# Performance work log

Hardware: AMD Instinct MI355X
Metric: run time of the kernel (lower is better)

The kernel has to match this reference:

```python
import jax, jax.numpy as jnp
import numpy as np
import math

FREQ_DIM = 161
OUTPUT_DIM = 4096
RNN_DIM = 128
EMBED_DIM = 32


def conv2d(x, w, b, stride):
    # x: (B, Cin, H, W), w: (Cout, Cin, kh, kw)
    out = jax.lax.conv_general_dilated(x, w, window_strides=stride, padding='VALID',
                                       dimension_numbers=('NCHW', 'OIHW', 'NCHW'))
    return out + b[None, :, None, None]


def gru_seq(x, w_ih, w_hh, b_ih, b_hh, h0):
    # x: (B, T, D); PyTorch GRU gate order: r, z, n
    B, T, D = x.shape
    H = h0.shape[-1]
    xg = jnp.einsum('btd,gd->btg', x, w_ih) + b_ih  # (B, T, 3H)

    def step(h, xg_t):
        hg = h @ w_hh.T + b_hh
        xr, xz, xn = jnp.split(xg_t, 3, axis=-1)
        hr, hz, hn = jnp.split(hg, 3, axis=-1)
        r = jax.nn.sigmoid(xr + hr)
        z = jax.nn.sigmoid(xz + hz)
        n = jnp.tanh(xn + r * hn)
        h_new = (1 - z) * n + z * h
        return h_new, h_new

    _, hs = jax.lax.scan(step, h0, jnp.swapaxes(xg, 0, 1))
    return jnp.swapaxes(hs, 0, 1)  # (B, T, H)


def gru_cell(ix, h, w_ih, w_hh, b_ih, b_hh):
    xg = ix @ w_ih.T + b_ih
    hg = h @ w_hh.T + b_hh
    xr, xz, xn = jnp.split(xg, 3, axis=-1)
    hr, hz, hn = jnp.split(hg, 3, axis=-1)
    r = jax.nn.sigmoid(xr + hr)
    z = jax.nn.sigmoid(xz + hz)
    n = jnp.tanh(xn + r * hn)
    return (1 - z) * n + z * h


def attend(eh, dhx):
    # eh: (B, T, H), dhx: (B, H)
    scores = jnp.einsum('bth,bh->bt', eh, dhx)
    a = jax.nn.softmax(scores, axis=-1)
    return jnp.einsum('bth,bt->bh', eh, a)


def setup_inputs() -> dict:
    key = jax.random.key(0)
    ks = jax.random.split(key, 16)

    def rn(k, shape, fan_in):
        s = 1.0 / math.sqrt(fan_in)
        return jax.random.uniform(k, shape, jnp.float32, -s, s)

    B, T_audio, L = 32, 512, 128
    x = jax.random.normal(ks[0], (B, T_audio, FREQ_DIM), jnp.float32)
    y = jax.random.randint(ks[1], (B, L), 0, OUTPUT_DIM)

    conv_in = 544  # 17 * 32 after two convs on freq dim 161
    params = {
        'conv1_w': rn(ks[2], (32, 1, 5, 32), 1 * 5 * 32),
        'conv1_b': rn(ks[3], (32,), 1 * 5 * 32),
        'conv2_w': rn(ks[4], (32, 32, 5, 32), 32 * 5 * 32),
        'conv2_b': rn(ks[5], (32,), 32 * 5 * 32),
        'rnn_w_ih': rn(ks[6], (3 * RNN_DIM, conv_in), RNN_DIM),
        'rnn_w_hh': rn(ks[7], (3 * RNN_DIM, RNN_DIM), RNN_DIM),
        'rnn_b_ih': rn(ks[8], (3 * RNN_DIM,), RNN_DIM),
        'rnn_b_hh': rn(ks[9], (3 * RNN_DIM,), RNN_DIM),
        'emb': jax.random.normal(ks[10], (OUTPUT_DIM, EMBED_DIM), jnp.float32),
        'dec_w_ih': rn(ks[11], (3 * RNN_DIM, EMBED_DIM), RNN_DIM),
        'dec_w_hh': rn(ks[12], (3 * RNN_DIM, RNN_DIM), RNN_DIM),
        'dec_b_ih': rn(ks[13], (3 * RNN_DIM,), RNN_DIM),
        'dec_b_hh': rn(ks[14], (3 * RNN_DIM,), RNN_DIM),
        'fc_w': rn(ks[15], (OUTPUT_DIM, RNN_DIM), RNN_DIM),
        'fc_b': rn(jax.random.fold_in(key, 99), (OUTPUT_DIM,), RNN_DIM),
        'h_init': jnp.zeros((1, RNN_DIM), jnp.float32),
    }
    return {'x': x, 'y': y, **params}


def forward(x, y, conv1_w, conv1_b, conv2_w, conv2_b,
            rnn_w_ih, rnn_w_hh, rnn_b_ih, rnn_b_hh,
            emb, dec_w_ih, dec_w_hh, dec_b_ih, dec_b_hh,
            fc_w, fc_b, h_init):
    B = x.shape[0]
    h = x[:, None, :, :]  # (B, 1, T, F)
    h = jax.nn.relu(conv2d(h, conv1_w, conv1_b, (2, 2)))
    h = jax.nn.relu(conv2d(h, conv2_w, conv2_b, (2, 2)))  # (B, 32, t, f)
    h = jnp.transpose(h, (0, 2, 3, 1))  # (B, t, f, c)
    b, t, f, c = h.shape
    h = h.reshape(b, t, f * c)
    eh = gru_seq(h, rnn_w_ih, rnn_w_hh, rnn_b_ih, rnn_b_hh,
                 jnp.zeros((b, RNN_DIM), h.dtype))  # (B, t, 128)

    inputs = emb[y[:, :-1]]  # (B, L-1, 32)
    hx = jnp.broadcast_to(h_init, (B, RNN_DIM))
    hx = hx + attend(eh, hx)

    def step(hx, ix):
        hx = gru_cell(ix, hx, dec_w_ih, dec_w_hh, dec_b_ih, dec_b_hh)
        hx = hx + attend(eh, hx)
        return hx, hx

    _, outs = jax.lax.scan(step, hx, jnp.swapaxes(inputs, 0, 1))
    out = jnp.concatenate([hx[:, None, :], jnp.swapaxes(outs, 0, 1)], axis=1)  # (B, L, 128)
    logits = jnp.einsum('btd,od->bto', out, fc_w) + fc_b
    return logits


def reference(x, y, conv1_w, conv1_b, conv2_w, conv2_b,
              rnn_w_ih, rnn_w_hh, rnn_b_ih, rnn_b_hh,
              emb, dec_w_ih, dec_w_hh, dec_b_ih, dec_b_hh,
              fc_w, fc_b, h_init):
    return forward(x, y, conv1_w, conv1_b, conv2_w, conv2_b,
                   rnn_w_ih, rnn_w_hh, rnn_b_ih, rnn_b_hh,
                   emb, dec_w_ih, dec_w_hh, dec_b_ih, dec_b_hh,
                   fc_w, fc_b, h_init)
```

## Files before the change

kernel.cpp:

```cpp
#include <hip/hip_runtime.h>
#include <stdint.h>

typedef unsigned short u16;
typedef uint32_t u32;

typedef __bf16 bf16x8 __attribute__((ext_vector_type(8)));
typedef float f32x4 __attribute__((ext_vector_type(4)));
typedef _Float16 h2v __attribute__((ext_vector_type(2)));

union B8 { uint4 q; u32 u[4]; bf16x8 v; };

__device__ __forceinline__ u16 f2bf(float f) {
  u32 u = __float_as_uint(f);
  u32 r = (u + 0x7fffu + ((u >> 16) & 1u)) >> 16;
  return (u16)r;
}
__device__ __forceinline__ u16 f2h(float f) {
  union { _Float16 h; u16 u; } v; v.h = (_Float16)f; return v.u;
}
__device__ __forceinline__ float dot2h(u32 a, u32 b, float c) {
  union U { u32 u; h2v v; } A, B; A.u = a; B.u = b;
  return __builtin_amdgcn_fdot2(A.v, B.v, c, false);
}
__device__ __forceinline__ float sigf(float x) { return 1.f / (1.f + __expf(-x)); }
__device__ __forceinline__ float tanhf_fast(float x) {
  x = fminf(fmaxf(x, -15.f), 15.f);
  float e = __expf(2.f * x);
  return (e - 1.f) / (e + 1.f);
}

__global__ __launch_bounds__(256) void prep_k(
    const float* rnn_w_hh, const float* dec_w_hh, const float* conv1_w,
    const float* conv2_w, const float* rnn_w_ih, const float* dec_w_ih,
    const float* fc_w, const float* emb, const int* y,
    u32* wT2e, u32* wT2d, u16* w1b, u16* w2b, u16* wihb, u16* dwihb,
    u16* fcwb, u16* adec)
{
  int e = blockIdx.x * 256 + threadIdx.x;
  const int S0 = 24576, S1 = 24576, S2 = 5120, S3 = 163840, S4 = 208896,
            S5 = 12288, S6 = 524288, S7 = 130048;
  if (e < S0) { int g = e >> 6, k2 = e & 63;
    wT2e[e] = (u32)f2h(rnn_w_hh[g*128 + 2*k2]) | ((u32)f2h(rnn_w_hh[g*128 + 2*k2 + 1]) << 16);
    return; }
  e -= S0;
  if (e < S1) { int g = e >> 6, k2 = e & 63;
    wT2d[e] = (u32)f2h(dec_w_hh[g*128 + 2*k2]) | ((u32)f2h(dec_w_hh[g*128 + 2*k2 + 1]) << 16);
    return; }
  e -= S1;
  if (e < S2) { int kh = e >> 10, c = (e >> 5) & 31, kw = e & 31;
    w1b[e] = f2bf(conv1_w[c*160 + kh*32 + kw]); return; }
  e -= S2;
  if (e < S3) { int kt = e >> 10, c = (e >> 5) & 31, kw = e & 31;
    int ic = kt / 5, kh = kt - ic * 5;
    w2b[e] = f2bf(conv2_w[((c*32 + ic)*5 + kh)*32 + kw]); return; }
  e -= S3;
  if (e < S4) { wihb[e] = f2bf(rnn_w_ih[e]); return; }
  e -= S4;
  if (e < S5) { dwihb[e] = f2bf(dec_w_ih[e]); return; }
  e -= S5;
  if (e < S6) { fcwb[e] = f2bf(fc_w[e]); return; }
  e -= S6;
  if (e < S7) { int m = e >> 5, k = e & 31;
    int b = m / 127, t = m - b * 127;
    adec[e] = f2bf(emb[y[b*128 + t]*32 + k]); return; }
}

__global__ __launch_bounds__(256) void conv1_k(const float* x, const u16* w1b,
                                               const float* c1b, u16* in1b)
{
  __shared__ __align__(16) u16 slab[35 * 162];
  __shared__ __align__(16) u16 wl[5120];
  int b = blockIdx.x >> 4;
  int oh0 = (blockIdx.x & 15) * 16;
  int ih0 = oh0 * 2;
  for (int e = threadIdx.x; e < 35 * 161; e += 256) {
    int r = e / 161, iw = e - r * 161;
    int ih = ih0 + r;
    float v = (ih < 512) ? x[(b*512 + ih)*161 + iw] : 0.f;
    slab[r*162 + iw] = f2bf(v);
  }
  for (int e = threadIdx.x; e < 5120; e += 256) wl[e] = w1b[e];
  __syncthreads();
  int lane = threadIdx.x & 63, wid = threadIdx.x >> 6;
  int lrow = lane & 15, lk = (lane >> 4) * 8;
  B8 bw[5][2];
  #pragma unroll
  for (int kt = 0; kt < 5; kt++)
    #pragma unroll
    for (int ct = 0; ct < 2; ct++)
      bw[kt][ct].q = *(const uint4*)&wl[(kt*32 + ct*16 + lrow)*32 + lk];
  float bias0 = c1b[lrow], bias1 = c1b[16 + lrow];
  for (int mt = wid; mt < 65; mt += 4) {
    int m = mt * 16 + lrow;
    int ohl = m / 65, ow = m - ohl * 65;
    int ro = ohl * 324 + ow * 2 + lk;
    f32x4 a0, a1;
    #pragma unroll
    for (int i = 0; i < 4; i++) { a0[i] = 0.f; a1[i] = 0.f; }
    #pragma unroll
    for (int kt = 0; kt < 5; kt++) {
      B8 af;
      const u32* p = (const u32*)&slab[ro + kt * 162];
      af.u[0] = p[0]; af.u[1] = p[1]; af.u[2] = p[2]; af.u[3] = p[3];
      a0 = __builtin_amdgcn_mfma_f32_16x16x32_bf16(af.v, bw[kt][0].v, a0, 0, 0, 0);
      a1 = __builtin_amdgcn_mfma_f32_16x16x32_bf16(af.v, bw[kt][1].v, a1, 0, 0, 0);
    }
    int rb = mt * 16 + (lane >> 4) * 4;
    #pragma unroll
    for (int i = 0; i < 4; i++) {
      int mr = rb + i;
      int ohl2 = mr / 65, ow2 = mr - ohl2 * 65;
      int oh = oh0 + ohl2;
      if (oh < 254) {
        float v0 = fmaxf(a0[i] + bias0, 0.f);
        float v1 = fmaxf(a1[i] + bias1, 0.f);
        in1b[((b*32 + lrow)*254 + oh)*72 + ow2] = f2bf(v0);
        in1b[((b*32 + 16 + lrow)*254 + oh)*72 + ow2] = f2bf(v1);
      }
    }
  }
}

__global__ __launch_bounds__(256) void conv2_k(const u16* in1b, const u16* w2b,
                                               const float* c2b, u16* hbf)
{
  extern __shared__ char smem[];
  u16* slab = (u16*)smem;
  u16* wl = (u16*)(smem + 87552);
  int b = blockIdx.x >> 4;
  int oh0 = (blockIdx.x & 15) * 8;
  int ih0 = oh0 * 2;
  for (int q = threadIdx.x; q < 5472; q += 256) {
    int ic = q / 171;
    int rem = q - ic * 171;
    int r = rem / 9, j = rem - r * 9;
    int ih = ih0 + r;
    uint4 v = make_uint4(0u, 0u, 0u, 0u);
    if (ih < 254) v = *(const uint4*)&in1b[(((b*32 + ic)*254 + ih)*72) + j*8];
    *(uint4*)&slab[(ic*19 + r)*72 + j*8] = v;
  }
  int lane = threadIdx.x & 63, wid = threadIdx.x >> 6;
  int lrow = lane & 15, lk = (lane >> 4) * 8;
  int ohl_[3], ow_[3];
  #pragma unroll
  for (int q = 0; q < 3; q++) {
    int mt = (q == 2) ? 8 : (wid + q * 4);
    int m = mt * 16 + lrow;
    if (m > 135) m = 0;
    ohl_[q] = m / 17; ow_[q] = m - ohl_[q] * 17;
  }
  f32x4 acc[3][2];
  #pragma unroll
  for (int q = 0; q < 3; q++)
    #pragma unroll
    for (int ct = 0; ct < 2; ct++)
      #pragma unroll
      for (int i = 0; i < 4; i++) acc[q][ct][i] = 0.f;

  for (int ph = 0; ph < 5; ph++) {
    __syncthreads();
    {
      const uint4* s4 = (const uint4*)&w2b[ph * 32768];
      uint4* d4 = (uint4*)wl;
      for (int q = threadIdx.x; q < 4096; q += 256) d4[q] = s4[q];
    }
    __syncthreads();
    for (int ktl = 0; ktl < 32; ktl++) {
      int ktg = ph * 32 + ktl;
      int ic = ktg / 5, kh = ktg - ic * 5;
      B8 fb0, fb1;
      fb0.q = *(const uint4*)&wl[(ktl*32 + lrow)*32 + lk];
      fb1.q = *(const uint4*)&wl[(ktl*32 + 16 + lrow)*32 + lk];
      int base = (ic * 19 + kh) * 72 + lk;
      #pragma unroll
      for (int q = 0; q < 3; q++) {
        if (q == 2 && wid != 0) break;
        B8 af;
        const u32* p = (const u32*)&slab[base + ohl_[q] * 144 + ow_[q] * 2];
        af.u[0] = p[0]; af.u[1] = p[1]; af.u[2] = p[2]; af.u[3] = p[3];
        acc[q][0] = __builtin_amdgcn_mfma_f32_16x16x32_bf16(af.v, fb0.v, acc[q][0], 0, 0, 0);
        acc[q][1] = __builtin_amdgcn_mfma_f32_16x16x32_bf16(af.v, fb1.v, acc[q][1], 0, 0, 0);
      }
    }
  }
  #pragma unroll
  for (int q = 0; q < 3; q++) {
    if (q == 2 && wid != 0) break;
    int mt = (q == 2) ? 8 : (wid + q * 4);
    int rb = mt * 16 + (lane >> 4) * 4;
    #pragma unroll
    for (int ct = 0; ct < 2; ct++) {
      int c = ct * 16 + lrow;
      float bias = c2b[c];
      #pragma unroll
      for (int i = 0; i < 4; i++) {
        int mr = rb + i;
        if (mr < 136) {
          int ohl = mr / 17, ow = mr - ohl * 17;
          int oh = oh0 + ohl;
          if (oh < 125) {
            float v = fmaxf(acc[q][ct][i] + bias, 0.f);
            hbf[(b*125 + oh)*544 + ow*32 + c] = f2bf(v);
          }
        }
      }
    }
  }
}

__global__ __launch_bounds__(256) void gemm_k(const u16* A, const u16* Bw,
                                              const float* bias, float* C,
                                              int M, int N, int K)
{
  __shared__ __align__(16) u16 As[64 * 32];
  __shared__ __align__(16) u16 Bs[64 * 32];
  int m0 = blockIdx.x * 64, n0 = blockIdx.y * 64;
  int tid = threadIdx.x;
  int lane = tid & 63, wid = tid >> 6;
  int lrow = lane & 15, lk = (lane >> 4) * 8;
  int sr = tid >> 2, sc8 = (tid & 3) * 8;
  f32x4 acc[4];
  #pragma unroll
  for (int nt = 0; nt < 4; nt++)
    #pragma unroll
    for (int i = 0; i < 4; i++) acc[nt][i] = 0.f;
  int nkt = K >> 5;
  for (int kt = 0; kt < nkt; kt++) {
    __syncthreads();
    uint4 va = make_uint4(0u, 0u, 0u, 0u);
    int arow = m0 + sr;
    if (arow < M) va = *(const uint4*)&A[arow * K + kt * 32 + sc8];
    *(uint4*)&As[sr * 32 + sc8] = va;
    uint4 vb = *(const uint4*)&Bw[(n0 + sr) * K + kt * 32 + sc8];
    *(uint4*)&Bs[sr * 32 + sc8] = vb;
    __syncthreads();
    B8 af; af.q = *(const uint4*)&As[(wid * 16 + lrow) * 32 + lk];
    #pragma unroll
    for (int nt = 0; nt < 4; nt++) {
      B8 bb; bb.q = *(const uint4*)&Bs[(nt * 16 + lrow) * 32 + lk];
      acc[nt] = __builtin_amdgcn_mfma_f32_16x16x32_bf16(af.v, bb.v, acc[nt], 0, 0, 0);
    }
  }
  #pragma unroll
  for (int nt = 0; nt < 4; nt++) {
    int col = n0 + nt * 16 + lrow;
    float bv = bias[col];
    #pragma unroll
    for (int i = 0; i < 4; i++) {
      int row = m0 + wid * 16 + (lane >> 4) * 4 + i;
      if (row < M) C[row * N + col] = acc[nt][i] + bv;
    }
  }
}

__global__ __launch_bounds__(1024, 1) void enc_k(const u32* wT2, const float* xg,
                                                 const float* bhh_g, u16* ehk, u16* eht)
{
  __shared__ __align__(16) u32 hp[2][2][64];
  __shared__ float hg[2][1152];
  int tid = threadIdx.x;
  int g = tid >> 9, tb = tid & 511, kh = tb >> 7, t = tb & 127;
  int b = blockIdx.x * 2 + g;
  u32 w0[16], w1[16], w2[16];
  {
    const uint4* p0 = (const uint4*)(wT2 + (size_t)t * 64 + kh * 16);
    const uint4* p1 = (const uint4*)(wT2 + (size_t)(128 + t) * 64 + kh * 16);
    const uint4* p2 = (const uint4*)(wT2 + (size_t)(256 + t) * 64 + kh * 16);
    #pragma unroll
    for (int j = 0; j < 4; j++) {
      uint4 q0 = p0[j]; w0[4*j] = q0.x; w0[4*j+1] = q0.y; w0[4*j+2] = q0.z; w0[4*j+3] = q0.w;
      uint4 q1 = p1[j]; w1[4*j] = q1.x; w1[4*j+1] = q1.y; w1[4*j+2] = q1.z; w1[4*j+3] = q1.w;
      uint4 q2 = p2[j]; w2[4*j] = q2.x; w2[4*j+1] = q2.y; w2[4*j+2] = q2.z; w2[4*j+3] = q2.w;
    }
  }
  float b0 = 0.f, b1 = 0.f, b2 = 0.f, xr0 = 0.f, xr1 = 0.f, xr2 = 0.f, hreg = 0.f;
  if (kh == 0) {
    b0 = bhh_g[t]; b1 = bhh_g[128 + t]; b2 = bhh_g[256 + t];
    const float* xp = &xg[(size_t)b * 125 * 384];
    xr0 = xp[t]; xr1 = xp[128 + t]; xr2 = xp[256 + t];
    ((u16*)&hp[g][0][0])[t] = 0;
  }
  __syncthreads();
  for (int tt = 0; tt < 125; tt++) {
    const u32* hb = &hp[g][tt & 1][kh * 16];
    float r0 = 0.f, r1 = 0.f, z0 = 0.f, z1 = 0.f, n0 = 0.f, n1 = 0.f;
    #pragma unroll
    for (int j = 0; j < 4; j++) {
      uint4 hv = *(const uint4*)&hb[4*j];
      r0 = dot2h(w0[4*j+0], hv.x, r0); r1 = dot2h(w0[4*j+1], hv.y, r1);
      r0 = dot2h(w0[4*j+2], hv.z, r0); r1 = dot2h(w0[4*j+3], hv.w, r1);
      z0 = dot2h(w1[4*j+0], hv.x, z0); z1 = dot2h(w1[4*j+1], hv.y, z1);
      z0 = dot2h(w1[4*j+2], hv.z, z0); z1 = dot2h(w1[4*j+3], hv.w, z1);
      n0 = dot2h(w2[4*j+0], hv.x, n0); n1 = dot2h(w2[4*j+1], hv.y, n1);
      n0 = dot2h(w2[4*j+2], hv.z, n0); n1 = dot2h(w2[4*j+3], hv.w, n1);
    }
    if (kh) {
      float* hh = &hg[g][(kh - 1) * 384];
      hh[t] = r0 + r1; hh[128 + t] = z0 + z1; hh[256 + t] = n0 + n1;
    }
    __syncthreads();
    if (kh == 0) {
      const float* hh = &hg[g][0];
      float pr = r0 + r1 + hh[t] + hh[384 + t] + hh[768 + t];
      float pz = z0 + z1 + hh[128 + t] + hh[512 + t] + hh[896 + t];
      float pn = n0 + n1 + hh[256 + t] + hh[640 + t] + hh[1024 + t];
      float r = sigf(xr0 + pr + b0);
      float z = sigf(xr1 + pz + b1);
      float n = tanhf_fast(xr2 + r * (pn + b2));
      hreg = (1.f - z) * n + z * hreg;
      u16 hv = f2h(hreg);
      ((u16*)&hp[g][(tt & 1) ^ 1][0])[t] = hv;
      ehk[((size_t)(b*64 + (t >> 1)) * 125 + tt) * 2 + (t & 1)] = hv;
      eht[((size_t)(b*128 + t)) * 128 + tt] = hv;
      if (tt + 1 < 125) {
        const float* xq = &xg[((size_t)b * 125 + tt + 1) * 384];
        xr0 = xq[t]; xr1 = xq[128 + t]; xr2 = xq[256 + t];
      }
    }
    __syncthreads();
  }
  if (kh == 0) {
    size_t rb = ((size_t)(b*128 + t)) * 128;
    eht[rb + 125] = 0; eht[rb + 126] = 0; eht[rb + 127] = 0;
  }
}

__global__ __launch_bounds__(1024, 1) void dec_k(const u32* wT2, const u32* ehk_g,
                                                 const u32* eht_g, const float* xgd,
                                                 const float* bhh_g, const float* h_init,
                                                 u16* outb)
{
  extern __shared__ char sm[];
  int tid = threadIdx.x;
  int g = tid >> 9, tb = tid & 511, kh = tb >> 7, t = tb & 127;
  int b = blockIdx.x * 2 + g;
  char* base = sm + (size_t)g * 41024;
  u32* elK   = (u32*)base;
  float* hgP = (float*)(base + 32000);
  float* sp  = (float*)(base + 36608);
  float* ctxB= (float*)(base + 38656);
  u16* hxA   = (u16*)(base + 40192);
  u16* hxB   = (u16*)(base + 40448);
  u16* scp   = (u16*)(base + 40704);
  float* red = (float*)(base + 40960);

  u32 w0[16], w1[16], w2[16];
  {
    const uint4* p0 = (const uint4*)(wT2 + (size_t)t * 64 + kh * 16);
    const uint4* p1 = (const uint4*)(wT2 + (size_t)(128 + t) * 64 + kh * 16);
    const uint4* p2 = (const uint4*)(wT2 + (size_t)(256 + t) * 64 + kh * 16);
    #pragma unroll
    for (int j = 0; j < 4; j++) {
      uint4 q0 = p0[j]; w0[4*j] = q0.x; w0[4*j+1] = q0.y; w0[4*j+2] = q0.z; w0[4*j+3] = q0.w;
      uint4 q1 = p1[j]; w1[4*j] = q1.x; w1[4*j+1] = q1.y; w1[4*j+2] = q1.z; w1[4*j+3] = q1.w;
      uint4 q2 = p2[j]; w2[4*j] = q2.x; w2[4*j+1] = q2.y; w2[4*j+2] = q2.z; w2[4*j+3] = q2.w;
    }
  }
  u32 rowr[16];
  {
    const uint4* rp = (const uint4*)(eht_g + (size_t)b * 8192 + (size_t)t * 64 + kh * 16);
    #pragma unroll
    for (int j = 0; j < 4; j++) {
      uint4 q = rp[j]; rowr[4*j] = q.x; rowr[4*j+1] = q.y; rowr[4*j+2] = q.z; rowr[4*j+3] = q.w;
    }
  }
  for (int e = tb; e < 8000; e += 512) elK[e] = ehk_g[(size_t)b * 8000 + e];
  float b0 = 0.f, b1 = 0.f, b2 = 0.f, xr0 = 0.f, xr1 = 0.f, xr2 = 0.f;
  float hxf = 0.f, hxg = 0.f;
  if (kh == 0) {
    b0 = bhh_g[t]; b1 = bhh_g[128 + t]; b2 = bhh_g[256 + t];
    hxf = h_init[t];
    const float* xp = &xgd[(size_t)b * 127 * 384];
    xr0 = xp[t]; xr1 = xp[128 + t]; xr2 = xp[256 + t];
  }
  __syncthreads();

  for (int step = 0; step < 128; step++) {
    if (step > 0) {
      const u32* hb = (const u32*)hxB + kh * 16;
      float r0 = 0.f, r1 = 0.f, z0 = 0.f, z1 = 0.f, n0 = 0.f, n1 = 0.f;
      #pragma unroll
      for (int j = 0; j < 4; j++) {
        uint4 hv = *(const uint4*)&hb[4*j];
        r0 = dot2h(w0[4*j+0], hv.x, r0); r1 = dot2h(w0[4*j+1], hv.y, r1);
        r0 = dot2h(w0[4*j+2], hv.z, r0); r1 = dot2h(w0[4*j+3], hv.w, r1);
        z0 = dot2h(w1[4*j+0], hv.x, z0); z1 = dot2h(w1[4*j+1], hv.y, z1);
        z0 = dot2h(w1[4*j+2], hv.z, z0); z1 = dot2h(w1[4*j+3], hv.w, z1);
        n0 = dot2h(w2[4*j+0], hv.x, n0); n1 = dot2h(w2[4*j+1], hv.y, n1);
        n0 = dot2h(w2[4*j+2], hv.z, n0); n1 = dot2h(w2[4*j+3], hv.w, n1);
      }
      if (kh) {
        float* hh = &hgP[(kh - 1) * 384];
        hh[t] = r0 + r1; hh[128 + t] = z0 + z1; hh[256 + t] = n0 + n1;
      }
      __syncthreads();
      if (kh == 0) {
        float pr = r0 + r1 + hgP[t] + hgP[384 + t] + hgP[768 + t];
        float pz = z0 + z1 + hgP[128 + t] + hgP[512 + t] + hgP[896 + t];
        float pn = n0 + n1 + hgP[256 + t] + hgP[640 + t] + hgP[1024 + t];
        float r = sigf(xr0 + pr + b0);
        float z = sigf(xr1 + pz + b1);
        float n = tanhf_fast(xr2 + r * (pn + b2));
        hxg = (1.f - z) * n + z * hxf;
        ((u16*)hxA)[t] = f2h(hxg);
        if (step < 127) {
          const float* xq = &xgd[((size_t)b * 127 + step) * 384];
          xr0 = xq[t]; xr1 = xq[128 + t]; xr2 = xq[256 + t];
        }
      }
      __syncthreads();
    } else {
      if (kh == 0) { hxg = hxf; ((u16*)hxA)[t] = f2h(hxg); }
      __syncthreads();
    }
    {
      float s0 = 0.f, s1 = 0.f;
      const u32* ek = &elK[(kh * 16) * 125];
      const u32* hxA4 = (const u32*)hxA;
      #pragma unroll
      for (int j = 0; j < 4; j++) {
        uint4 aw = *(const uint4*)&hxA4[kh * 16 + 4*j];
        s0 = dot2h(ek[(4*j+0)*125 + t], aw.x, s0);
        s1 = dot2h(ek[(4*j+1)*125 + t], aw.y, s1);
        s0 = dot2h(ek[(4*j+2)*125 + t], aw.z, s0);
        s1 = dot2h(ek[(4*j+3)*125 + t], aw.w, s1);
      }
      sp[kh * 128 + t] = s0 + s1;
    }
    __syncthreads();
    if (kh == 0) {
      float s = (t < 125) ? (sp[t] + sp[128 + t] + sp[256 + t] + sp[384 + t]) : -1e30f;
      float mw = s;
      #pragma unroll
      for (int o = 32; o > 0; o >>= 1) mw = fmaxf(mw, __shfl_xor(mw, o));
      float ev = (t < 125) ? __expf(s - mw) : 0.f;
      float sw = ev;
      #pragma unroll
      for (int o = 32; o > 0; o >>= 1) sw += __shfl_xor(sw, o);
      ((u16*)scp)[t] = f2h(ev);
      if ((t & 63) == 0) { int wv = t >> 6; red[wv*2] = mw; red[wv*2 + 1] = sw; }
    }
    __syncthreads();
    float m0r = red[0], S0r = red[1], m1r = red[2], S1r = red[3];
    float M = fmaxf(m0r, m1r);
    float f0 = __expf(m0r - M), f1 = __expf(m1r - M);
    float inv = 1.f / (f0 * S0r + f1 * S1r);
    float c0 = 0.f, c1 = 0.f;
    {
      const u32* scp4 = (const u32*)scp;
      #pragma unroll
      for (int j = 0; j < 4; j++) {
        uint4 sw4 = *(const uint4*)&scp4[kh * 16 + 4*j];
        c0 = dot2h(rowr[4*j+0], sw4.x, c0); c1 = dot2h(rowr[4*j+1], sw4.y, c1);
        c0 = dot2h(rowr[4*j+2], sw4.z, c0); c1 = dot2h(rowr[4*j+3], sw4.w, c1);
      }
    }
    if (kh) ctxB[(kh - 1) * 128 + t] = c0 + c1;
    __syncthreads();
    if (kh == 0) {
      float ctx = ((c0 + c1) + ctxB[t]) * f0 + (ctxB[128 + t] + ctxB[256 + t]) * f1;
      hxf = hxg + ctx * inv;
      outb[((size_t)(b * 128) + step) * 128 + t] = f2bf(hxf);
      ((u16*)hxB)[t] = f2h(hxf);
    }
    __syncthreads();
  }
}

extern "C" void kernel_launch(void* const* d_in, const int* in_sizes, int n_in,
                              void* d_out, int out_size, void* d_ws, size_t ws_size,
                              hipStream_t stream)
{
  const float* x        = (const float*)d_in[0];
  const int*   y        = (const int*)d_in[1];
  const float* conv1_w  = (const float*)d_in[2];
  const float* conv1_b  = (const float*)d_in[3];
  const float* conv2_w  = (const float*)d_in[4];
  const float* conv2_b  = (const float*)d_in[5];
  const float* rnn_w_ih = (const float*)d_in[6];
  const float* rnn_w_hh = (const float*)d_in[7];
  const float* rnn_b_ih = (const float*)d_in[8];
  const float* rnn_b_hh = (const float*)d_in[9];
  const float* emb      = (const float*)d_in[10];
  const float* dec_w_ih = (const float*)d_in[11];
  const float* dec_w_hh = (const float*)d_in[12];
  const float* dec_b_ih = (const float*)d_in[13];
  const float* dec_b_hh = (const float*)d_in[14];
  const float* fc_w     = (const float*)d_in[15];
  const float* fc_b     = (const float*)d_in[16];
  const float* h_init   = (const float*)d_in[17];
  float* logits = (float*)d_out;

  char* ws = (char*)d_ws;
  size_t off = 0;
  auto alloc = [&](size_t bytes) { char* p = ws + off; off = (off + bytes + 255) & ~(size_t)255; return p; };
  u16* in1b  = (u16*)alloc(37453824);
  u16* hbf   = (u16*)alloc(4352000);
  float* xge = (float*)alloc(6144000);
  u32* ehb_k = (u32*)alloc(1024000);
  u32* ehb_t = (u32*)alloc(1048576);
  float* xgd = (float*)alloc(6242304);
  u16* adec  = (u16*)alloc(260096);
  u16* outb  = (u16*)alloc(1048576);
  u32* wT2e  = (u32*)alloc(98304);
  u32* wT2d  = (u32*)alloc(98304);
  u16* w1b   = (u16*)alloc(10240);
  u16* w2b   = (u16*)alloc(327680);
  u16* wihb  = (u16*)alloc(417792);
  u16* dwihb = (u16*)alloc(24576);
  u16* fcwb  = (u16*)alloc(1048576);

  hipFuncSetAttribute((const void*)conv2_k, hipFuncAttributeMaxDynamicSharedMemorySize, 153088);
  hipFuncSetAttribute((const void*)dec_k,   hipFuncAttributeMaxDynamicSharedMemorySize, 82048);

  prep_k<<<4272, 256, 0, stream>>>(rnn_w_hh, dec_w_hh, conv1_w, conv2_w, rnn_w_ih,
                                   dec_w_ih, fc_w, emb, y,
                                   wT2e, wT2d, w1b, w2b, wihb, dwihb, fcwb, adec);
  conv1_k<<<512, 256, 0, stream>>>(x, w1b, conv1_b, in1b);
  conv2_k<<<512, 256, 153088, stream>>>(in1b, w2b, conv2_b, hbf);
  gemm_k<<<dim3(63, 6), 256, 0, stream>>>(hbf, wihb, rnn_b_ih, xge, 4000, 384, 544);
  gemm_k<<<dim3(64, 6), 256, 0, stream>>>(adec, dwihb, dec_b_ih, xgd, 4064, 384, 32);
  enc_k<<<16, 1024, 0, stream>>>(wT2e, xge, rnn_b_hh, (u16*)ehb_k, (u16*)ehb_t);
  dec_k<<<16, 1024, 82048, stream>>>(wT2d, ehb_k, ehb_t, xgd, dec_b_hh, h_init, outb);
  gemm_k<<<dim3(64, 64), 256, 0, stream>>>(outb, fcwb, fc_b, logits, 4096, 4096, 128);
}
```

Before: 604.0 us.

## Retile conv2 for more blocks, add dedicated FC GEMM, grid-stride prep kernel

conv2 now processes 4 output rows per block instead of 8 and stages weights in 10-row phases, which halves shared memory and doubles the block count to raise occupancy. The final logits projection moves from the generic 64x64 GEMM to a specialised 128x64 tile kernel that reuses B fragments across two M sub-tiles. The prep kernel processes four elements per thread with a quarter of the blocks. Smaller conv2 tiles add halo reloads and more weight-staging syncs.

After: 601.7 us (median of 2 runs). Within noise of the previous version (-0.4%).

```diff
diff --git a/kernel.cpp b/kernel.cpp
--- a/kernel.cpp
+++ b/kernel.cpp
@@ -29,14 +29,13 @@
   return (e - 1.f) / (e + 1.f);
 }
 
-__global__ __launch_bounds__(256) void prep_k(
+__device__ __forceinline__ void prep_one(int e,
     const float* rnn_w_hh, const float* dec_w_hh, const float* conv1_w,
     const float* conv2_w, const float* rnn_w_ih, const float* dec_w_ih,
     const float* fc_w, const float* emb, const int* y,
     u32* wT2e, u32* wT2d, u16* w1b, u16* w2b, u16* wihb, u16* dwihb,
     u16* fcwb, u16* adec)
 {
-  int e = blockIdx.x * 256 + threadIdx.x;
   const int S0 = 24576, S1 = 24576, S2 = 5120, S3 = 163840, S4 = 208896,
             S5 = 12288, S6 = 524288, S7 = 130048;
   if (e < S0) { int g = e >> 6, k2 = e & 63;
@@ -65,6 +64,23 @@
     adec[e] = f2bf(emb[y[b*128 + t]*32 + k]); return; }
 }
 
+__global__ __launch_bounds__(256) void prep_k(
+    const float* rnn_w_hh, const float* dec_w_hh, const float* conv1_w,
+    const float* conv2_w, const float* rnn_w_ih, const float* dec_w_ih,
+    const float* fc_w, const float* emb, const int* y,
+    u32* wT2e, u32* wT2d, u16* w1b, u16* w2b, u16* wihb, u16* dwihb,
+    u16* fcwb, u16* adec)
+{
+  int e0 = blockIdx.x * 256 + threadIdx.x;
+  #pragma unroll
+  for (int it = 0; it < 4; it++) {
+    int e = e0 + it * 273408;
+    if (e < 1093632)
+      prep_one(e, rnn_w_hh, dec_w_hh, conv1_w, conv2_w, rnn_w_ih, dec_w_ih,
+               fc_w, emb, y, wT2e, wT2d, w1b, w2b, wihb, dwihb, fcwb, adec);
+  }
+}
+
 __global__ __launch_bounds__(256) void conv1_k(const float* x, const u16* w1b,
                                                const float* c1b, u16* in1b)
 {
@@ -126,55 +142,56 @@
 {
   extern __shared__ char smem[];
   u16* slab = (u16*)smem;
-  u16* wl = (u16*)(smem + 87552);
-  int b = blockIdx.x >> 4;
-  int oh0 = (blockIdx.x & 15) * 8;
+  u16* wl = (u16*)(smem + 50688);
+  int b = blockIdx.x >> 5;
+  int tile = blockIdx.x & 31;
+  int oh0 = tile * 4;
   int ih0 = oh0 * 2;
-  for (int q = threadIdx.x; q < 5472; q += 256) {
-    int ic = q / 171;
-    int rem = q - ic * 171;
+  for (int q = threadIdx.x; q < 3168; q += 256) {
+    int ic = q / 99;
+    int rem = q - ic * 99;
     int r = rem / 9, j = rem - r * 9;
     int ih = ih0 + r;
     uint4 v = make_uint4(0u, 0u, 0u, 0u);
     if (ih < 254) v = *(const uint4*)&in1b[(((b*32 + ic)*254 + ih)*72) + j*8];
-    *(uint4*)&slab[(ic*19 + r)*72 + j*8] = v;
+    *(uint4*)&slab[(ic*11 + r)*72 + j*8] = v;
   }
   int lane = threadIdx.x & 63, wid = threadIdx.x >> 6;
   int lrow = lane & 15, lk = (lane >> 4) * 8;
-  int ohl_[3], ow_[3];
-  #pragma unroll
-  for (int q = 0; q < 3; q++) {
-    int mt = (q == 2) ? 8 : (wid + q * 4);
+  int ohl_[2], ow_[2];
+  #pragma unroll
+  for (int q = 0; q < 2; q++) {
+    int mt = (q == 1) ? 4 : wid;
     int m = mt * 16 + lrow;
-    if (m > 135) m = 0;
+    if (m > 67) m = 0;
     ohl_[q] = m / 17; ow_[q] = m - ohl_[q] * 17;
   }
-  f32x4 acc[3][2];
-  #pragma unroll
-  for (int q = 0; q < 3; q++)
+  f32x4 acc[2][2];
+  #pragma unroll
+  for (int q = 0; q < 2; q++)
     #pragma unroll
     for (int ct = 0; ct < 2; ct++)
       #pragma unroll
       for (int i = 0; i < 4; i++) acc[q][ct][i] = 0.f;
 
-  for (int ph = 0; ph < 5; ph++) {
+  for (int ph = 0; ph < 16; ph++) {
     __syncthreads();
     {
-      const uint4* s4 = (const uint4*)&w2b[ph * 32768];
+      const uint4* s4 = (const uint4*)&w2b[ph * 10240];
       uint4* d4 = (uint4*)wl;
-      for (int q = threadIdx.x; q < 4096; q += 256) d4[q] = s4[q];
-    }
-    __syncthreads();
-    for (int ktl = 0; ktl < 32; ktl++) {
-      int ktg = ph * 32 + ktl;
+      for (int q = threadIdx.x; q < 1280; q += 256) d4[q] = s4[q];
+    }
+    __syncthreads();
+    for (int ktl = 0; ktl < 10; ktl++) {
+      int ktg = ph * 10 + ktl;
       int ic = ktg / 5, kh = ktg - ic * 5;
       B8 fb0, fb1;
       fb0.q = *(const uint4*)&wl[(ktl*32 + lrow)*32 + lk];
       fb1.q = *(const uint4*)&wl[(ktl*32 + 16 + lrow)*32 + lk];
-      int base = (ic * 19 + kh) * 72 + lk;
-      #pragma unroll
-      for (int q = 0; q < 3; q++) {
-        if (q == 2 && wid != 0) break;
+      int base = (ic * 11 + kh) * 72 + lk;
+      #pragma unroll
+      for (int q = 0; q < 2; q++) {
+        if (q == 1 && wid != 0) break;
         B8 af;
         const u32* p = (const u32*)&slab[base + ohl_[q] * 144 + ow_[q] * 2];
         af.u[0] = p[0]; af.u[1] = p[1]; af.u[2] = p[2]; af.u[3] = p[3];
@@ -184,9 +201,9 @@
     }
   }
   #pragma unroll
-  for (int q = 0; q < 3; q++) {
-    if (q == 2 && wid != 0) break;
-    int mt = (q == 2) ? 8 : (wid + q * 4);
+  for (int q = 0; q < 2; q++) {
+    if (q == 1 && wid != 0) break;
+    int mt = (q == 1) ? 4 : wid;
     int rb = mt * 16 + (lane >> 4) * 4;
     #pragma unroll
     for (int ct = 0; ct < 2; ct++) {
@@ -195,7 +212,7 @@
       #pragma unroll
       for (int i = 0; i < 4; i++) {
         int mr = rb + i;
-        if (mr < 136) {
+        if (mr < 68) {
           int ohl = mr / 17, ow = mr - ohl * 17;
           int oh = oh0 + ohl;
           if (oh < 125) {
@@ -250,6 +267,60 @@
       int row = m0 + wid * 16 + (lane >> 4) * 4 + i;
       if (row < M) C[row * N + col] = acc[nt][i] + bv;
     }
+  }
+}
+
+__global__ __launch_bounds__(256) void fc_k(const u16* A, const u16* Bw,
+                                            const float* bias, float* C)
+{
+  __shared__ __align__(16) u16 As[128 * 32];
+  __shared__ __align__(16) u16 Bs[64 * 32];
+  int m0 = blockIdx.x * 128, n0 = blockIdx.y * 64;
+  int tid = threadIdx.x;
+  int lane = tid & 63, wid = tid >> 6;
+  int lrow = lane & 15, lk = (lane >> 4) * 8;
+  f32x4 acc[2][4];
+  #pragma unroll
+  for (int mq = 0; mq < 2; mq++)
+    #pragma unroll
+    for (int nt = 0; nt < 4; nt++)
+      #pragma unroll
+      for (int i = 0; i < 4; i++) acc[mq][nt][i] = 0.f;
+  #pragma unroll
+  for (int kt = 0; kt < 4; kt++) {
+    __syncthreads();
+    #pragma unroll
+    for (int i = tid; i < 512; i += 256) {
+      int row = i >> 2, q = i & 3;
+      *(uint4*)&As[row * 32 + q * 8] = *(const uint4*)&A[(m0 + row) * 128 + kt * 32 + q * 8];
+    }
+    {
+      int row = tid >> 2, q = tid & 3;
+      *(uint4*)&Bs[row * 32 + q * 8] = *(const uint4*)&Bw[(n0 + row) * 128 + kt * 32 + q * 8];
+    }
+    __syncthreads();
+    B8 bb[4];
+    #pragma unroll
+    for (int nt = 0; nt < 4; nt++) bb[nt].q = *(const uint4*)&Bs[(nt * 16 + lrow) * 32 + lk];
+    #pragma unroll
+    for (int mq = 0; mq < 2; mq++) {
+      B8 af; af.q = *(const uint4*)&As[((wid * 2 + mq) * 16 + lrow) * 32 + lk];
+      #pragma unroll
+      for (int nt = 0; nt < 4; nt++)
+        acc[mq][nt] = __builtin_amdgcn_mfma_f32_16x16x32_bf16(af.v, bb[nt].v, acc[mq][nt], 0, 0, 0);
+    }
+  }
+  #pragma unroll
+  for (int nt = 0; nt < 4; nt++) {
+    int col = n0 + nt * 16 + lrow;
+    float bv = bias[col];
+    #pragma unroll
+    for (int mq = 0; mq < 2; mq++)
+      #pragma unroll
+      for (int i = 0; i < 4; i++) {
+        int row = m0 + (wid * 2 + mq) * 16 + (lane >> 4) * 4 + i;
+        C[(size_t)row * 4096 + col] = acc[mq][nt][i] + bv;
+      }
   }
 }
 
@@ -510,17 +581,17 @@
   u16* dwihb = (u16*)alloc(24576);
   u16* fcwb  = (u16*)alloc(1048576);
 
-  hipFuncSetAttribute((const void*)conv2_k, hipFuncAttributeMaxDynamicSharedMemorySize, 153088);
+  hipFuncSetAttribute((const void*)conv2_k, hipFuncAttributeMaxDynamicSharedMemorySize, 71168);
   hipFuncSetAttribute((const void*)dec_k,   hipFuncAttributeMaxDynamicSharedMemorySize, 82048);
 
-  prep_k<<<4272, 256, 0, stream>>>(rnn_w_hh, dec_w_hh, conv1_w, conv2_w, rnn_w_ih,
+  prep_k<<<1068, 256, 0, stream>>>(rnn_w_hh, dec_w_hh, conv1_w, conv2_w, rnn_w_ih,
                                    dec_w_ih, fc_w, emb, y,
                                    wT2e, wT2d, w1b, w2b, wihb, dwihb, fcwb, adec);
   conv1_k<<<512, 256, 0, stream>>>(x, w1b, conv1_b, in1b);
-  conv2_k<<<512, 256, 153088, stream>>>(in1b, w2b, conv2_b, hbf);
+  conv2_k<<<1024, 256, 71168, stream>>>(in1b, w2b, conv2_b, hbf);
   gemm_k<<<dim3(63, 6), 256, 0, stream>>>(hbf, wihb, rnn_b_ih, xge, 4000, 384, 544);
   gemm_k<<<dim3(64, 6), 256, 0, stream>>>(adec, dwihb, dec_b_ih, xgd, 4064, 384, 32);
   enc_k<<<16, 1024, 0, stream>>>(wT2e, xge, rnn_b_hh, (u16*)ehb_k, (u16*)ehb_t);
   dec_k<<<16, 1024, 82048, stream>>>(wT2d, ehb_k, ehb_t, xgd, dec_b_hh, h_init, outb);
-  gemm_k<<<dim3(64, 64), 256, 0, stream>>>(outb, fcwb, fc_b, logits, 4096, 4096, 128);
-}
+  fc_k<<<dim3(32, 64), 256, 0, stream>>>(outb, fcwb, fc_b, logits);
+}
```
